# Kernel optimization log

Hardware: AMD Instinct MI355X
Metric: run time of the kernel (lower is better)

The kernel has to match this reference:

```python
import jax, jax.numpy as jnp
import numpy as np

B_SZ, L, H, N = 2, 2048, 128, 64
EPS = 1e-12


def setup_inputs() -> dict:
    key = jax.random.key(0)
    ks = jax.random.split(key, 6)
    u = jax.random.normal(ks[0], (B_SZ, L, H), dtype=jnp.float32)
    # parameters mimicking the layer's initialization structure
    log_A_real = jnp.log(0.5 * jnp.ones((H, N), dtype=jnp.float32))
    A_imag = (np.pi * jnp.broadcast_to(jnp.arange(N, dtype=jnp.float32), (H, N))).astype(jnp.float32)
    Bp = jax.random.normal(ks[1], (H, N, 2), dtype=jnp.float32)
    log_dt = (jax.random.uniform(ks[2], (1,)) * (jnp.log(0.1) - jnp.log(0.001)) + jnp.log(0.001)).astype(jnp.float32)
    C = (jax.random.normal(ks[3], (1, N, 2), dtype=jnp.float32) * (0.5 ** 0.5)).astype(jnp.float32)
    D = jnp.ones((H,), dtype=jnp.float32)
    return {"u": u, "log_A_real": log_A_real, "A_imag": A_imag, "B": Bp,
            "log_dt": log_dt, "C": C, "D": D}


def reference(u, log_A_real, A_imag, B, log_dt, C, D):
    # discretized diagonal SSM (S4D / ZOH-like): Lambda [H,N] complex
    Lam = jax.lax.complex(-jnp.exp(log_A_real), A_imag)            # [H,N] complex64
    Bc = jax.lax.complex(B[..., 0], B[..., 1])                     # [H,N]
    Cc = jax.lax.complex(C[0, :, 0], C[0, :, 1])                   # [N]
    step = jnp.exp(log_dt)[0].astype(jnp.complex64)                # scalar
    dA = Lam * step                                                 # [H,N]
    dB = Bc * (jnp.exp(dA) - 1.0) / Lam                            # [H,N]

    # selective_scan (non-stateful branch).
    # dA is constant over (b, l), so the padded/shifted cumsum of dA along l
    # equals t * dA at position t; exp of it is the decay prefix product.
    t = jnp.arange(L, dtype=jnp.float32)                           # [L]
    dA_cumsum = jnp.exp(dA[None, None, :, :] * t[None, :, None, None].astype(jnp.complex64))  # [1,L,H,N]

    dB_u = u[..., None].astype(jnp.complex64) * dB[None, None]     # [B,L,H,N]
    x = jnp.cumsum(dB_u / (dA_cumsum + EPS), axis=1) * dA_cumsum   # [B,L,H,N]
    y = jnp.einsum('bldn,n->bld', x, Cc)                           # [B,L,H] complex
    # original adds real u*D to y; output is the real signal
    return jnp.real(y) + u * D[None, None, :]
```

## Files before the change

### kernel.cpp

```cpp
#include <hip/hip_runtime.h>
#include <hip/hip_fp16.h>
#include <math.h>

#define BB 2
#define LL 2048
#define HH 128
#define NN 64
#define LCH 32
#define NCHT (LL/LCH)
#define WPB 8
#define EPSF 1e-12f
#define ROWPH 70
#define UP 9

__device__ __forceinline__ float bcast(float v, int idx) {
  return __int_as_float(__builtin_amdgcn_readlane(__float_as_int(v), idx));
}

extern "C" __global__ __launch_bounds__(256)
void s4d_prep(const float* __restrict__ lar, const float* __restrict__ aim,
              const float* __restrict__ ldt, const float* __restrict__ Cp,
              float2* __restrict__ gcT, float2* __restrict__ pA,
              float2* __restrict__ pQ, float2* __restrict__ pQ16)
{
  int tid = blockIdx.x * 256 + threadIdx.x;
  int n = tid & 63;
  int t = tid >> 6;
  float dt  = expf(ldt[0]);
  float lre = -expf(lar[n]);
  float w   = aim[n];
  float ar = lre * dt, ai = w * dt;
  float er = expf(ar);
  float s, c; sincosf(ai, &s, &c);
  float aa = er * c - 1.0f, bb = er * s;
  float il2 = 1.0f / (lre*lre + w*w);
  float qr = (aa*lre + bb*w) * il2;
  float qi = (bb*lre - aa*w) * il2;
  float cr = Cp[n*2+0], ci = Cp[n*2+1];
  float cqr = cr*qr - ci*qi, cqi = cr*qi + ci*qr;
  float tf = (float)t;
  float rho = expf(ar * tf);
  float s2, c2; sincosf(ai * tf, &s2, &c2);
  float zr = rho * c2, zi = rho * s2;
  float dr = zr + EPSF;
  float den = fmaf(dr, dr, zi*zi);
  float inv = 1.0f / den;
  float gr = fmaf(zr, dr, zi*zi) * inv;
  float gi = (zi*dr - zr*zi) * inv;
  gcT[tid] = make_float2(cqr*gr - cqi*gi, cqr*gi + cqi*gr);
  if (blockIdx.x == 0 && threadIdx.x < 64) {
    pA[n] = make_float2(er * c, er * s);
    float rq = expf(ar * (float)LCH);
    float sq, cq; sincosf(ai * (float)LCH, &sq, &cq);
    pQ[n] = make_float2(rq * cq, rq * sq);
    float r16 = expf(ar * (float)(LCH*16));
    float s16, c16; sincosf(ai * (float)(LCH*16), &s16, &c16);
    pQ16[n] = make_float2(r16 * c16, r16 * s16);
  }
}

__device__ __forceinline__ void load_u_tile(
    float* lds_ut, const float* __restrict__ u, int b, int c, int h0, int tid)
{
  if (tid < 256) {
    int k = tid >> 3, hh = tid & 7;
    lds_ut[k*UP + hh] = u[((size_t)b*LL + c*LCH + k)*HH + h0 + hh];
  }
}

extern "C" __global__ __launch_bounds__(512)
void s4d_k1(const float* __restrict__ u, const float* __restrict__ Bp,
            const float2* __restrict__ pA, const float2* __restrict__ gcT,
            float2* __restrict__ states)
{
  __shared__ float2 gs[LCH * NN];
  __shared__ float lds_ut[LCH * UP];
  int tid = threadIdx.x;
  int lane = tid & 63;
  int wv   = tid >> 6;
  int c  = blockIdx.x & (NCHT-1);
  int hg = (blockIdx.x >> 6) & (HH/WPB - 1);
  int b  = blockIdx.x >> 10;
  int h  = hg * WPB + wv;

  const float4* gsrc = reinterpret_cast<const float4*>(gcT + (size_t)c * LCH * NN);
  float4* gdst = reinterpret_cast<float4*>(gs);
  #pragma unroll
  for (int i = 0; i < 2; ++i)
    gdst[tid + 512*i] = gsrc[tid + 512*i];
  load_u_tile(lds_ut, u, b, c, hg*WPB, tid);

  float2 a2 = pA[lane];
  float2 Bc = *reinterpret_cast<const float2*>(Bp + (size_t)(h*NN + lane)*2);
  __syncthreads();

  float ureg = lds_ut[(lane & 31)*UP + wv];

  float pr = 0.f, pi = 0.f;
  #pragma unroll
  for (int k = 0; k < LCH; ++k) {
    float2 g = gs[k*NN + lane];
    float uv = bcast(ureg, k);
    float kgr = fmaf(Bc.x, g.x, -Bc.y*g.y);
    float kgi = fmaf(Bc.x, g.y,  Bc.y*g.x);
    float prn = fmaf(a2.x, pr, fmaf(-a2.y, pi, uv*kgr));
    float pin = fmaf(a2.y, pr, fmaf( a2.x, pi, uv*kgi));
    pr = prn; pi = pin;
  }
  states[(((size_t)b*HH + h)*NCHT + c)*NN + lane] = make_float2(pr, pi);
}

extern "C" __global__ __launch_bounds__(256)
void s4d_k2(const float2* __restrict__ pQ, const float2* __restrict__ pQ16,
            float2* __restrict__ states)
{
  __shared__ float2 st[NCHT * 64];
  __shared__ float2 Ssum[4 * 64];
  int bh = blockIdx.x;
  size_t base = (size_t)bh * NCHT * 64;

  #pragma unroll 4
  for (int k = threadIdx.x; k < NCHT*64; k += 256)
    st[k] = states[base + k];
  __syncthreads();

  int n = threadIdx.x & 63, q = threadIdx.x >> 6;
  float2 A = pQ[n];

  float2 x = make_float2(0.f, 0.f);
  #pragma unroll 4
  for (int j = 0; j < 16; ++j) {
    int cc = 16*q + j;
    float2 tmp = st[cc*64 + n];
    st[cc*64 + n] = x;
    float xrn = fmaf(A.x, x.x, fmaf(-A.y, x.y, tmp.x));
    float xin = fmaf(A.y, x.x, fmaf( A.x, x.y, tmp.y));
    x = make_float2(xrn, xin);
  }
  Ssum[q*64 + n] = x;
  __syncthreads();

  if (threadIdx.x < 64) {
    float2 Aq = pQ16[n];
    float2 X = make_float2(0.f, 0.f);
    #pragma unroll
    for (int p = 0; p < 4; ++p) {
      float2 tmp = Ssum[p*64 + n];
      Ssum[p*64 + n] = X;
      float xrn = fmaf(Aq.x, X.x, fmaf(-Aq.y, X.y, tmp.x));
      float xin = fmaf(Aq.y, X.x, fmaf( Aq.x, X.y, tmp.y));
      X = make_float2(xrn, xin);
    }
  }
  __syncthreads();

  float2 carry = Ssum[q*64 + n];
  float2 Ap = make_float2(1.f, 0.f);
  #pragma unroll 4
  for (int j = 0; j < 16; ++j) {
    int cc = 16*q + j;
    float2 v = st[cc*64 + n];
    v.x = fmaf(Ap.x, carry.x, fmaf(-Ap.y, carry.y, v.x));
    v.y = fmaf(Ap.x, carry.y, fmaf( Ap.y, carry.x, v.y));
    st[cc*64 + n] = v;
    float apr = Ap.x*A.x - Ap.y*A.y;
    float api = Ap.x*A.y + Ap.y*A.x;
    Ap = make_float2(apr, api);
  }
  __syncthreads();

  #pragma unroll 4
  for (int k = threadIdx.x; k < NCHT*64; k += 256)
    states[base + k] = st[k];
}

extern "C" __global__ __launch_bounds__(512)
void s4d_k3(const float* __restrict__ u, const float* __restrict__ Bp,
            const float2* __restrict__ pA, const float2* __restrict__ gcT,
            const float* __restrict__ Dp, const float2* __restrict__ states,
            float* __restrict__ out)
{
  __shared__ float2 gs[LCH * NN];
  __shared__ ushort tile[WPB * LCH * ROWPH];
  __shared__ float lds_ut[LCH * UP];
  int tid = threadIdx.x;
  int lane = tid & 63;
  int wv   = tid >> 6;
  int c  = blockIdx.x & (NCHT-1);
  int hg = (blockIdx.x >> 6) & (HH/WPB - 1);
  int b  = blockIdx.x >> 10;
  int h  = hg * WPB + wv;
  ushort* myl = tile + wv * (LCH * ROWPH);

  const float4* gsrc = reinterpret_cast<const float4*>(gcT + (size_t)c * LCH * NN);
  float4* gdst = reinterpret_cast<float4*>(gs);
  #pragma unroll
  for (int i = 0; i < 2; ++i)
    gdst[tid + 512*i] = gsrc[tid + 512*i];
  load_u_tile(lds_ut, u, b, c, hg*WPB, tid);

  float2 cin = states[(((size_t)b*HH + h)*NCHT + c)*NN + lane];
  float2 a2 = pA[lane];
  float2 Bc = *reinterpret_cast<const float2*>(Bp + (size_t)(h*NN + lane)*2);
  float Dh = Dp[h];
  __syncthreads();

  float ureg = lds_ut[(lane & 31)*UP + wv];

  float pr = cin.x, pi = cin.y;
  #pragma unroll
  for (int k = 0; k < LCH; ++k) {
    float2 g = gs[k*NN + lane];
    float uv = bcast(ureg, k);
    float kgr = fmaf(Bc.x, g.x, -Bc.y*g.y);
    float kgi = fmaf(Bc.x, g.y,  Bc.y*g.x);
    float prn = fmaf(a2.x, pr, fmaf(-a2.y, pi, uv*kgr));
    float pin = fmaf(a2.y, pr, fmaf( a2.x, pi, uv*kgi));
    pr = prn; pi = pin;
    myl[k * ROWPH + lane] = __half_as_ushort(__float2half(pr));
  }

  __builtin_amdgcn_s_waitcnt(0);

  int m = lane & 31, hf = lane >> 5;
  const ushort* rowp = myl + m * ROWPH + hf * 32;
  float s = 0.f;
  #pragma unroll
  for (int j = 0; j < 16; ++j) {
    unsigned int v = *reinterpret_cast<const unsigned int*>(rowp + 2*j);
    float2 f = __half22float2(*reinterpret_cast<const __half2*>(&v));
    s += f.x + f.y;
  }
  s += __shfl_xor(s, 32);
  if (lane < 32) {
    float uv = lds_ut[m*UP + wv];
    out[((size_t)b*LL + c*LCH + m)*HH + h] = s + uv * Dh;
  }
}

extern "C" void kernel_launch(void* const* d_in, const int* in_sizes, int n_in,
                              void* d_out, int out_size, void* d_ws, size_t ws_size,
                              hipStream_t stream)
{
  const float* u   = (const float*)d_in[0];
  const float* lar = (const float*)d_in[1];
  const float* aim = (const float*)d_in[2];
  const float* Bp  = (const float*)d_in[3];
  const float* ldt = (const float*)d_in[4];
  const float* Cp  = (const float*)d_in[5];
  const float* Dp  = (const float*)d_in[6];
  float* out = (float*)d_out;

  auto alignup = [](size_t x) { return (x + 255) & ~(size_t)255; };
  size_t sz_states = (size_t)BB*HH*NCHT*NN*sizeof(float2);
  size_t sz_gc  = (size_t)LL*NN*sizeof(float2);
  size_t sz_64  = (size_t)NN*sizeof(float2);

  char* wp = (char*)d_ws;
  float2* states = (float2*)wp;  wp += alignup(sz_states);
  float2* gcT    = (float2*)wp;  wp += alignup(sz_gc);
  float2* pA     = (float2*)wp;  wp += alignup(sz_64);
  float2* pQ     = (float2*)wp;  wp += alignup(sz_64);
  float2* pQ16   = (float2*)wp;  wp += alignup(sz_64);
  (void)ws_size;

  s4d_prep<<<dim3(512), dim3(256), 0, stream>>>(lar, aim, ldt, Cp, gcT, pA, pQ, pQ16);
  s4d_k1<<<dim3(BB*(HH/WPB)*NCHT), dim3(512), 0, stream>>>(u, Bp, pA, gcT, states);
  s4d_k2<<<dim3(BB*HH), dim3(256), 0, stream>>>(pQ, pQ16, states);
  s4d_k3<<<dim3(BB*(HH/WPB)*NCHT), dim3(512), 0, stream>>>(u, Bp, pA, gcT, Dp, states, out);
}
```

Before: 45.20 us.

## Split chunk output into local scan plus carry-in correction with decay powers

```diff
diff --git a/kernel.cpp b/kernel.cpp
--- a/kernel.cpp
+++ b/kernel.cpp
@@ -21,41 +21,55 @@
 void s4d_prep(const float* __restrict__ lar, const float* __restrict__ aim,
               const float* __restrict__ ldt, const float* __restrict__ Cp,
               float2* __restrict__ gcT, float2* __restrict__ pA,
-              float2* __restrict__ pQ, float2* __restrict__ pQ16)
-{
-  int tid = blockIdx.x * 256 + threadIdx.x;
-  int n = tid & 63;
-  int t = tid >> 6;
-  float dt  = expf(ldt[0]);
-  float lre = -expf(lar[n]);
-  float w   = aim[n];
-  float ar = lre * dt, ai = w * dt;
-  float er = expf(ar);
-  float s, c; sincosf(ai, &s, &c);
-  float aa = er * c - 1.0f, bb = er * s;
-  float il2 = 1.0f / (lre*lre + w*w);
-  float qr = (aa*lre + bb*w) * il2;
-  float qi = (bb*lre - aa*w) * il2;
-  float cr = Cp[n*2+0], ci = Cp[n*2+1];
-  float cqr = cr*qr - ci*qi, cqi = cr*qi + ci*qr;
-  float tf = (float)t;
-  float rho = expf(ar * tf);
-  float s2, c2; sincosf(ai * tf, &s2, &c2);
-  float zr = rho * c2, zi = rho * s2;
-  float dr = zr + EPSF;
-  float den = fmaf(dr, dr, zi*zi);
-  float inv = 1.0f / den;
-  float gr = fmaf(zr, dr, zi*zi) * inv;
-  float gi = (zi*dr - zr*zi) * inv;
-  gcT[tid] = make_float2(cqr*gr - cqi*gi, cqr*gi + cqi*gr);
-  if (blockIdx.x == 0 && threadIdx.x < 64) {
-    pA[n] = make_float2(er * c, er * s);
-    float rq = expf(ar * (float)LCH);
-    float sq, cq; sincosf(ai * (float)LCH, &sq, &cq);
-    pQ[n] = make_float2(rq * cq, rq * sq);
-    float r16 = expf(ar * (float)(LCH*16));
-    float s16, c16; sincosf(ai * (float)(LCH*16), &s16, &c16);
-    pQ16[n] = make_float2(r16 * c16, r16 * s16);
+              float2* __restrict__ pQ, float2* __restrict__ pQ16,
+              float2* __restrict__ apow)
+{
+  if (blockIdx.x < 512) {
+    int tid = blockIdx.x * 256 + threadIdx.x;
+    int n = tid & 63;
+    int t = tid >> 6;
+    float dt  = expf(ldt[0]);
+    float lre = -expf(lar[n]);
+    float w   = aim[n];
+    float ar = lre * dt, ai = w * dt;
+    float er = expf(ar);
+    float s, c; sincosf(ai, &s, &c);
+    float aa = er * c - 1.0f, bb = er * s;
+    float il2 = 1.0f / (lre*lre + w*w);
+    float qr = (aa*lre + bb*w) * il2;
+    float qi = (bb*lre - aa*w) * il2;
+    float cr = Cp[n*2+0], ci = Cp[n*2+1];
+    float cqr = cr*qr - ci*qi, cqi = cr*qi + ci*qr;
+    float tf = (float)t;
+    float rho = expf(ar * tf);
+    float s2, c2; sincosf(ai * tf, &s2, &c2);
+    float zr = rho * c2, zi = rho * s2;
+    float dr = zr + EPSF;
+    float den = fmaf(dr, dr, zi*zi);
+    float inv = 1.0f / den;
+    float gr = fmaf(zr, dr, zi*zi) * inv;
+    float gi = (zi*dr - zr*zi) * inv;
+    gcT[tid] = make_float2(cqr*gr - cqi*gi, cqr*gi + cqi*gr);
+    if (blockIdx.x == 0 && threadIdx.x < 64) {
+      pA[n] = make_float2(er * c, er * s);
+      float rq = expf(ar * (float)LCH);
+      float sq, cq; sincosf(ai * (float)LCH, &sq, &cq);
+      pQ[n] = make_float2(rq * cq, rq * sq);
+      float r16 = expf(ar * (float)(LCH*16));
+      float s16, c16; sincosf(ai * (float)(LCH*16), &s16, &c16);
+      pQ16[n] = make_float2(r16 * c16, r16 * s16);
+    }
+  } else {
+    int tid2 = (blockIdx.x - 512) * 256 + threadIdx.x;
+    int n = tid2 & 63;
+    int d = tid2 >> 6;
+    float dt  = expf(ldt[0]);
+    float lre = -expf(lar[n]);
+    float w   = aim[n];
+    float ar = lre * dt, ai = w * dt;
+    float e = expf(ar * (float)(d + 1));
+    float s, c; sincosf(ai * (float)(d + 1), &s, &c);
+    apow[tid2] = make_float2(e * c, e * s);
   }
 }
 
@@ -69,11 +83,13 @@
 }
 
 extern "C" __global__ __launch_bounds__(512)
-void s4d_k1(const float* __restrict__ u, const float* __restrict__ Bp,
+void s4d_kS(const float* __restrict__ u, const float* __restrict__ Bp,
             const float2* __restrict__ pA, const float2* __restrict__ gcT,
-            float2* __restrict__ states)
+            const float* __restrict__ Dp,
+            float2* __restrict__ states, float* __restrict__ y0T)
 {
   __shared__ float2 gs[LCH * NN];
+  __shared__ ushort tile[WPB * LCH * ROWPH];
   __shared__ float lds_ut[LCH * UP];
   int tid = threadIdx.x;
   int lane = tid & 63;
@@ -82,6 +98,7 @@
   int hg = (blockIdx.x >> 6) & (HH/WPB - 1);
   int b  = blockIdx.x >> 10;
   int h  = hg * WPB + wv;
+  ushort* myl = tile + wv * (LCH * ROWPH);
 
   const float4* gsrc = reinterpret_cast<const float4*>(gcT + (size_t)c * LCH * NN);
   float4* gdst = reinterpret_cast<float4*>(gs);
@@ -92,6 +109,7 @@
 
   float2 a2 = pA[lane];
   float2 Bc = *reinterpret_cast<const float2*>(Bp + (size_t)(h*NN + lane)*2);
+  float Dh = Dp[h];
   __syncthreads();
 
   float ureg = lds_ut[(lane & 31)*UP + wv];
@@ -106,8 +124,27 @@
     float prn = fmaf(a2.x, pr, fmaf(-a2.y, pi, uv*kgr));
     float pin = fmaf(a2.y, pr, fmaf( a2.x, pi, uv*kgi));
     pr = prn; pi = pin;
-  }
+    myl[k * ROWPH + lane] = __half_as_ushort(__float2half(pr));
+  }
+
   states[(((size_t)b*HH + h)*NCHT + c)*NN + lane] = make_float2(pr, pi);
+
+  __builtin_amdgcn_s_waitcnt(0);
+
+  int m = lane & 31, hf = lane >> 5;
+  const ushort* rowp = myl + m * ROWPH + hf * 32;
+  float s = 0.f;
+  #pragma unroll
+  for (int j = 0; j < 16; ++j) {
+    unsigned int v = *reinterpret_cast<const unsigned int*>(rowp + 2*j);
+    float2 f = __half22float2(*reinterpret_cast<const __half2*>(&v));
+    s += f.x + f.y;
+  }
+  s += __shfl_xor(s, 32);
+  if (lane < 32) {
+    float uv = lds_ut[m*UP + wv];
+    y0T[((size_t)b*HH + h)*LL + c*LCH + m] = s + uv * Dh;
+  }
 }
 
 extern "C" __global__ __launch_bounds__(256)
@@ -175,14 +212,11 @@
 }
 
 extern "C" __global__ __launch_bounds__(512)
-void s4d_k3(const float* __restrict__ u, const float* __restrict__ Bp,
-            const float2* __restrict__ pA, const float2* __restrict__ gcT,
-            const float* __restrict__ Dp, const float2* __restrict__ states,
-            float* __restrict__ out)
-{
-  __shared__ float2 gs[LCH * NN];
+void s4d_kC(const float2* __restrict__ apow, const float2* __restrict__ states,
+            const float* __restrict__ y0T, float* __restrict__ out)
+{
+  __shared__ float2 apw[LCH * NN];
   __shared__ ushort tile[WPB * LCH * ROWPH];
-  __shared__ float lds_ut[LCH * UP];
   int tid = threadIdx.x;
   int lane = tid & 63;
   int wv   = tid >> 6;
@@ -192,37 +226,34 @@
   int h  = hg * WPB + wv;
   ushort* myl = tile + wv * (LCH * ROWPH);
 
-  const float4* gsrc = reinterpret_cast<const float4*>(gcT + (size_t)c * LCH * NN);
-  float4* gdst = reinterpret_cast<float4*>(gs);
+  const float4* asrc = reinterpret_cast<const float4*>(apow);
+  float4* adst = reinterpret_cast<float4*>(apw);
   #pragma unroll
   for (int i = 0; i < 2; ++i)
-    gdst[tid + 512*i] = gsrc[tid + 512*i];
-  load_u_tile(lds_ut, u, b, c, hg*WPB, tid);
-
-  float2 cin = states[(((size_t)b*HH + h)*NCHT + c)*NN + lane];
-  float2 a2 = pA[lane];
-  float2 Bc = *reinterpret_cast<const float2*>(Bp + (size_t)(h*NN + lane)*2);
-  float Dh = Dp[h];
-  __syncthreads();
-
-  float ureg = lds_ut[(lane & 31)*UP + wv];
-
-  float pr = cin.x, pi = cin.y;
-  #pragma unroll
-  for (int k = 0; k < LCH; ++k) {
-    float2 g = gs[k*NN + lane];
-    float uv = bcast(ureg, k);
-    float kgr = fmaf(Bc.x, g.x, -Bc.y*g.y);
-    float kgi = fmaf(Bc.x, g.y,  Bc.y*g.x);
-    float prn = fmaf(a2.x, pr, fmaf(-a2.y, pi, uv*kgr));
-    float pin = fmaf(a2.y, pr, fmaf( a2.x, pi, uv*kgi));
-    pr = prn; pi = pin;
-    myl[k * ROWPH + lane] = __half_as_ushort(__float2half(pr));
+    adst[tid + 512*i] = asrc[tid + 512*i];
+
+  float2 C = states[(((size_t)b*HH + h)*NCHT + c)*NN + lane];
+  float y0v = y0T[((size_t)b*HH + h)*LL + c*LCH + (lane & 31)];
+  __syncthreads();
+
+  size_t obase = ((size_t)b*LL + c*LCH) * HH + h;
+  int m = lane & 31;
+
+  if (__all(fabsf(C.x) + fabsf(C.y) < 1e-4f)) {
+    if (lane < 32) out[obase + (size_t)m*HH] = y0v;
+    return;
+  }
+
+  #pragma unroll
+  for (int d = 0; d < LCH; ++d) {
+    float2 a = apw[d*NN + lane];
+    float val = fmaf(a.x, C.x, -a.y*C.y);
+    myl[d * ROWPH + lane] = __half_as_ushort(__float2half(val));
   }
 
   __builtin_amdgcn_s_waitcnt(0);
 
-  int m = lane & 31, hf = lane >> 5;
+  int hf = lane >> 5;
   const ushort* rowp = myl + m * ROWPH + hf * 32;
   float s = 0.f;
   #pragma unroll
@@ -232,10 +263,8 @@
     s += f.x + f.y;
   }
   s += __shfl_xor(s, 32);
-  if (lane < 32) {
-    float uv = lds_ut[m*UP + wv];
-    out[((size_t)b*LL + c*LCH + m)*HH + h] = s + uv * Dh;
-  }
+  if (lane < 32)
+    out[obase + (size_t)m*HH] = y0v + s;
 }
 
 extern "C" void kernel_launch(void* const* d_in, const int* in_sizes, int n_in,
@@ -254,18 +283,22 @@
   auto alignup = [](size_t x) { return (x + 255) & ~(size_t)255; };
   size_t sz_states = (size_t)BB*HH*NCHT*NN*sizeof(float2);
   size_t sz_gc  = (size_t)LL*NN*sizeof(float2);
+  size_t sz_y0  = (size_t)BB*HH*LL*sizeof(float);
+  size_t sz_ap  = (size_t)LCH*NN*sizeof(float2);
   size_t sz_64  = (size_t)NN*sizeof(float2);
 
   char* wp = (char*)d_ws;
   float2* states = (float2*)wp;  wp += alignup(sz_states);
   float2* gcT    = (float2*)wp;  wp += alignup(sz_gc);
+  float*  y0T    = (float*)wp;   wp += alignup(sz_y0);
+  float2* apow   = (float2*)wp;  wp += alignup(sz_ap);
   float2* pA     = (float2*)wp;  wp += alignup(sz_64);
   float2* pQ     = (float2*)wp;  wp += alignup(sz_64);
   float2* pQ16   = (float2*)wp;  wp += alignup(sz_64);
   (void)ws_size;
 
-  s4d_prep<<<dim3(512), dim3(256), 0, stream>>>(lar, aim, ldt, Cp, gcT, pA, pQ, pQ16);
-  s4d_k1<<<dim3(BB*(HH/WPB)*NCHT), dim3(512), 0, stream>>>(u, Bp, pA, gcT, states);
+  s4d_prep<<<dim3(520), dim3(256), 0, stream>>>(lar, aim, ldt, Cp, gcT, pA, pQ, pQ16, apow);
+  s4d_kS<<<dim3(BB*(HH/WPB)*NCHT), dim3(512), 0, stream>>>(u, Bp, pA, gcT, Dp, states, y0T);
   s4d_k2<<<dim3(BB*HH), dim3(256), 0, stream>>>(pQ, pQ16, states);
-  s4d_k3<<<dim3(BB*(HH/WPB)*NCHT), dim3(512), 0, stream>>>(u, Bp, pA, gcT, Dp, states, out);
-}
+  s4d_kC<<<dim3(BB*(HH/WPB)*NCHT), dim3(512), 0, stream>>>(apow, states, y0T, out);
+}
```

After: 45.30 us. About the same (+0.2%).
